# Kernel tuning notes

Hardware: AMD Instinct MI355X
Metric: run time of the kernel (lower is better)

Reference implementation:

```python
import jax, jax.numpy as jnp
import numpy as np

N = 100000   # nodes
E = 220000   # directed edges (each branch)
H = 128      # hidden_dim
OUT = 1      # output_dim
G = 4096     # num graphs in batch
PE = 5       # laplacian eigenvector PE dims
VOCAB = 28   # atom types


def gcn_conv(x, src, dst, W, b, n):
    # PyG GCNConv: x' = D^-1/2 (A + I) D^-1/2 (X W) + b
    h = x @ W
    deg = jax.ops.segment_sum(jnp.ones(src.shape[0], x.dtype), dst, num_segments=n) + 1.0
    dinv = jax.lax.rsqrt(deg)
    coef = dinv[src] * dinv[dst]                                    # [E]
    agg = jax.ops.segment_sum(h[src] * coef[:, None], dst, num_segments=n)
    agg = agg + h * (dinv * dinv)[:, None]                          # self-loop term
    return agg + b


def gcn2(x, edge_index, W1, b1, W2, b2, n):
    # PyG GCN model, num_layers=2: conv -> relu -> conv
    src, dst = edge_index[0], edge_index[1]
    h = jax.nn.relu(gcn_conv(x, src, dst, W1, b1, n))
    return gcn_conv(h, src, dst, W2, b2, n)


def setup_inputs() -> dict:
    key = jax.random.key(0)
    ks = jax.random.split(key, 16)
    s = 0.1
    return {
        "node_tokens": jax.random.randint(ks[0], (N, 1), 0, VOCAB),
        "pe": jax.random.normal(ks[1], (N, PE), jnp.float32),
        "edge_index": jax.random.randint(ks[2], (2, E), 0, N),
        "vr_edge_index": jax.random.randint(ks[3], (2, E), 0, N),
        "batch": jnp.sort(jax.random.randint(ks[4], (N,), 0, G)),
        "embed_table": jax.random.normal(ks[5], (VOCAB, H), jnp.float32) * s,
        "Wt": jax.random.normal(ks[6], (PE, H), jnp.float32) * s,
        "bt": jnp.zeros((H,), jnp.float32),
        "W1": jax.random.normal(ks[7], (H, H), jnp.float32) * s,
        "b1": jnp.zeros((H,), jnp.float32),
        "W2": jax.random.normal(ks[8], (H, OUT), jnp.float32) * s,
        "b2": jnp.zeros((OUT,), jnp.float32),
        "Wv1": jax.random.normal(ks[9], (H, H), jnp.float32) * s,
        "bv1": jnp.zeros((H,), jnp.float32),
        "Wv2": jax.random.normal(ks[10], (H, OUT), jnp.float32) * s,
        "bv2": jnp.zeros((OUT,), jnp.float32),
    }


def reference(node_tokens, pe, edge_index, vr_edge_index, batch, embed_table,
              Wt, bt, W1, b1, W2, b2, Wv1, bv1, Wv2, bv2):
    # embed_x(data.x.long()).squeeze(1) + lin_trans(pe)
    x = embed_table[node_tokens[:, 0]] + (pe @ Wt + bt)             # [N, H]
    x1 = gcn2(x, edge_index, W1, b1, W2, b2, N)                     # [N, OUT]
    xv = gcn2(x, vr_edge_index, Wv1, bv1, Wv2, bv2, N)              # [N, OUT]
    x1 = x1 + xv
    y_hat = jax.ops.segment_sum(x1, batch, num_segments=G)          # [G, OUT]
    y_hat = jnp.squeeze(y_hat, axis=-1)                             # [G]
    return (y_hat, x)
```

## Files before the change

### kernel.cpp

```cpp
#include <hip/hip_runtime.h>

#define NN 100000
#define NE 220000
#define HD 128
#define NG 4096
#define NPE 5
#define NB_SCAN ((NN + 255) / 256)
#define NBX4 ((NN * HD / 4) / 256)
#define NBF ((NN + 127) / 128)
#define NBW 128
#define NBZ ((2 * NN + 255) / 256)
#define NBE2 14
#define NBD ((2 * NE + 255) / 256)
#define LDP 136

typedef unsigned int uint;
typedef unsigned short ushort;
typedef __attribute__((ext_vector_type(8))) short bf16x8;
typedef __attribute__((ext_vector_type(4))) float f32x4;

__device__ __forceinline__ float bf2f(uint u16) {
    return __uint_as_float(u16 << 16);
}
__device__ __forceinline__ ushort f2bf(float f) {
    uint u = __float_as_uint(f);
    u += 0x7fffu + ((u >> 16) & 1u);
    return (ushort)(u >> 16);
}

__global__ void k_prep0(const float* __restrict__ W1, const float* __restrict__ Wv1,
                        const float* __restrict__ embed, const float* __restrict__ bt,
                        ushort* __restrict__ Wcat, int* __restrict__ cnt,
                        float* __restrict__ embed2) {
    int b = blockIdx.x;
    if (b < NBW) {
        int t = b * 256 + threadIdx.x;
        int f = t >> 7, k = t & 127;
        const float* W = (f < HD) ? W1 : Wv1;
        Wcat[t] = f2bf(W[k * HD + (f & 127)]);
    } else if (b < NBW + NBZ) {
        int t = (b - NBW) * 256 + threadIdx.x;
        if (t < 2 * NN) cnt[t] = 0;
    } else {
        int t = (b - NBW - NBZ) * 256 + threadIdx.x;
        if (t < 28 * 128) embed2[t] = embed[t] + bt[t & 127];
    }
}

__global__ void k_front(const int* __restrict__ tok, const float* __restrict__ pe,
                        const float* __restrict__ embed2, const float* __restrict__ Wtr,
                        float* __restrict__ x, ushort* __restrict__ xb,
                        const int* __restrict__ ei, const int* __restrict__ vei,
                        int* __restrict__ cnt) {
    int b = blockIdx.x;
    if (b < NBX4) {
        int idx = b * 256 + threadIdx.x;
        int n = idx >> 5, q = idx & 31;
        int t = tok[n];
        float4 acc = ((const float4*)(embed2 + (size_t)t * HD))[q];
        const float* pen = pe + n * NPE;
#pragma unroll
        for (int k = 0; k < NPE; ++k) {
            float p = pen[k];
            float4 wv = ((const float4*)(Wtr + k * HD))[q];
            acc.x += p * wv.x; acc.y += p * wv.y;
            acc.z += p * wv.z; acc.w += p * wv.w;
        }
        ((float4*)x)[idx] = acc;
        uint2 pk;
        pk.x = (uint)f2bf(acc.x) | ((uint)f2bf(acc.y) << 16);
        pk.y = (uint)f2bf(acc.z) | ((uint)f2bf(acc.w) << 16);
        ((uint2*)xb)[idx] = pk;
    } else {
        int t = (b - NBX4) * 256 + threadIdx.x;
        if (t < 2 * NE) {
            int br = t >= NE;
            int e = t - br * NE;
            const int* S = br ? vei : ei;
            atomicAdd(&cnt[br * NN + S[NE + e]], 1);
        }
    }
}

__global__ __launch_bounds__(256) void k_gemm(const ushort* __restrict__ xb,
                                              const ushort* __restrict__ Wt,
                                              ushort* __restrict__ H) {
    __shared__ ushort As[128 * LDP];
    int bi = blockIdx.x;
    int fh = bi >= NBF;
    int n0 = (bi - fh * NBF) * 128;
    int tid = threadIdx.x;
    {
        uint4* dst = (uint4*)As;
        for (int i = tid; i < 2048; i += 256) {
            int n = n0 + (i >> 4);
            uint4 v = {0u, 0u, 0u, 0u};
            if (n < NN) v = ((const uint4*)(xb + (size_t)n * HD))[i & 15];
            dst[(i >> 4) * 17 + (i & 15)] = v;
        }
    }
    __syncthreads();
    int w = tid >> 6, lane = tid & 63;
    int m = lane & 15, quad = lane >> 4;
    const ushort* Wg = Wt + (size_t)fh * 128 * 128;
    f32x4 acc[2][8] = {};
#pragma unroll
    for (int kc = 0; kc < 4; ++kc) {
        int k0 = kc * 32 + quad * 8;
        bf16x8 xf[2];
#pragma unroll
        for (int nt = 0; nt < 2; ++nt)
            xf[nt] = *(const bf16x8*)&As[((w * 2 + nt) * 16 + m) * LDP + k0];
#pragma unroll
        for (int ft = 0; ft < 8; ++ft) {
            bf16x8 wf = *(const bf16x8*)&Wg[(ft * 16 + m) * 128 + k0];
#pragma unroll
            for (int nt = 0; nt < 2; ++nt)
                acc[nt][ft] = __builtin_amdgcn_mfma_f32_16x16x32_bf16(
                    wf, xf[nt], acc[nt][ft], 0, 0, 0);
        }
    }
#pragma unroll
    for (int nt = 0; nt < 2; ++nt) {
        int n = n0 + (w * 2 + nt) * 16 + m;
        if (n >= NN) continue;
#pragma unroll
        for (int ft = 0; ft < 8; ++ft) {
            f32x4 a = acc[nt][ft];
            uint2 pk;
            pk.x = (uint)f2bf(a[0]) | ((uint)f2bf(a[1]) << 16);
            pk.y = (uint)f2bf(a[2]) | ((uint)f2bf(a[3]) << 16);
            *(uint2*)&H[(size_t)n * 256 + fh * 128 + ft * 16 + quad * 4] = pk;
        }
    }
}

__global__ void k_scan1(const int* __restrict__ cnt, int* __restrict__ off,
                        int* __restrict__ bsum, float* __restrict__ dinv,
                        float* __restrict__ y) {
    __shared__ int s[256];
    int tid = threadIdx.x;
    int gid = blockIdx.x * 256 + tid;
    if (gid < NG) y[gid] = 0.f;
    int br = blockIdx.x / NB_SCAN;
    int blk = blockIdx.x % NB_SCAN;
    int i = blk * 256 + tid;
    int v = (i < NN) ? cnt[br * NN + i] : 0;
    if (i < NN) dinv[br * NN + i] = rsqrtf((float)v + 1.0f);
    s[tid] = v;
    __syncthreads();
    for (int d = 1; d < 256; d <<= 1) {
        int t = (tid >= d) ? s[tid - d] : 0;
        __syncthreads();
        s[tid] += t;
        __syncthreads();
    }
    if (i < NN) off[br * NN + i] = s[tid] - v;
    if (tid == 255) bsum[br * 512 + blk] = s[255];
}

__global__ void k_scan2(int* __restrict__ bsum) {
    __shared__ int s[512];
    int br = blockIdx.x;
    int tid = threadIdx.x;
    int v = (tid < NB_SCAN) ? bsum[br * 512 + tid] : 0;
    s[tid] = v;
    __syncthreads();
    for (int d = 1; d < 512; d <<= 1) {
        int t = (tid >= d) ? s[tid - d] : 0;
        __syncthreads();
        s[tid] += t;
        __syncthreads();
    }
    if (tid < NB_SCAN) bsum[br * 512 + tid] = s[tid] - v;
}

__global__ void k_scan3(const int* __restrict__ off, const int* __restrict__ bsum,
                        const int* __restrict__ cnt, int2* __restrict__ off2,
                        int* __restrict__ cur) {
    int br = blockIdx.x / NB_SCAN;
    int blk = blockIdx.x % NB_SCAN;
    int i = blk * 256 + threadIdx.x;
    if (i < NN) {
        int o = off[br * NN + i] + bsum[br * 512 + blk];
        int2 pr;
        pr.x = o;
        pr.y = o + cnt[br * NN + i];
        off2[br * NN + i] = pr;
        cur[br * NN + i] = o;
    }
}

__global__ void k_scatter(const int* __restrict__ ei, const int* __restrict__ vei,
                          const float* __restrict__ dinv, int* __restrict__ cur,
                          int2* __restrict__ ent) {
    int t = blockIdx.x * blockDim.x + threadIdx.x;
    if (t >= 2 * NE) return;
    int br = t >= NE;
    int e = t - br * NE;
    const int* S = br ? vei : ei;
    int s = S[e], d = S[NE + e];
    int pos = atomicAdd(&cur[br * NN + d], 1);
    int2 rec;
    rec.x = s;
    rec.y = __float_as_int(dinv[br * NN + s] * dinv[br * NN + d]);
    ent[br * NE + pos] = rec;
}

__global__ void k_gather_ep(const ushort* __restrict__ H, const float* __restrict__ dinv,
                            const int2* __restrict__ off2,
                            const int2* __restrict__ ent,
                            const float* __restrict__ b1, const float* __restrict__ bv1,
                            const float* __restrict__ W2, const float* __restrict__ Wv2,
                            float* __restrict__ z) {
    int wid = threadIdx.x >> 6;
    int lane = threadIdx.x & 63;
    int half = lane >> 5;
    int l = lane & 31;
    int task = blockIdx.x * 8 + wid * 2 + half;
    int br = task >= NN;
    int n = task - br * NN;

    const int2* en = ent + br * NE;
    size_t hoff = (size_t)br * 128;

    float dv = dinv[br * NN + n];
    uint2 u = *(const uint2*)(H + (size_t)n * 256 + hoff + l * 4);
    float c = dv * dv;
    float a0 = bf2f(u.x & 0xffffu) * c, a1 = bf2f(u.x >> 16) * c;
    float a2 = bf2f(u.y & 0xffffu) * c, a3 = bf2f(u.y >> 16) * c;

    int2 pr = off2[br * NN + n];
    int p0 = pr.x, p1 = pr.y;
    for (int p = p0; p < p1; p += 4) {
        int2 e0 = en[p], e1 = en[p + 1], e2 = en[p + 2], e3 = en[p + 3];
        int s0 = e0.x;
        int s1 = (p + 1 < p1) ? e1.x : n;
        int s2 = (p + 2 < p1) ? e2.x : n;
        int s3 = (p + 3 < p1) ? e3.x : n;
        float c0 = __int_as_float(e0.y);
        float c1 = (p + 1 < p1) ? __int_as_float(e1.y) : 0.f;
        float c2 = (p + 2 < p1) ? __int_as_float(e2.y) : 0.f;
        float c3 = (p + 3 < p1) ? __int_as_float(e3.y) : 0.f;
        uint2 v0 = *(const uint2*)(H + (size_t)s0 * 256 + hoff + l * 4);
        uint2 v1 = *(const uint2*)(H + (size_t)s1 * 256 + hoff + l * 4);
        uint2 v2 = *(const uint2*)(H + (size_t)s2 * 256 + hoff + l * 4);
        uint2 v3 = *(const uint2*)(H + (size_t)s3 * 256 + hoff + l * 4);
        a0 += bf2f(v0.x & 0xffffu) * c0; a1 += bf2f(v0.x >> 16) * c0;
        a2 += bf2f(v0.y & 0xffffu) * c0; a3 += bf2f(v0.y >> 16) * c0;
        a0 += bf2f(v1.x & 0xffffu) * c1; a1 += bf2f(v1.x >> 16) * c1;
        a2 += bf2f(v1.y & 0xffffu) * c1; a3 += bf2f(v1.y >> 16) * c1;
        a0 += bf2f(v2.x & 0xffffu) * c2; a1 += bf2f(v2.x >> 16) * c2;
        a2 += bf2f(v2.y & 0xffffu) * c2; a3 += bf2f(v2.y >> 16) * c2;
        a0 += bf2f(v3.x & 0xffffu) * c3; a1 += bf2f(v3.x >> 16) * c3;
        a2 += bf2f(v3.y & 0xffffu) * c3; a3 += bf2f(v3.y >> 16) * c3;
    }

    const float* bb = br ? bv1 : b1;
    const float* ww = br ? Wv2 : W2;
    float4 b4 = *(const float4*)&bb[l * 4];
    float4 w4 = *(const float4*)&ww[l * 4];
    float part = fmaxf(a0 + b4.x, 0.f) * w4.x + fmaxf(a1 + b4.y, 0.f) * w4.y
               + fmaxf(a2 + b4.z, 0.f) * w4.z + fmaxf(a3 + b4.w, 0.f) * w4.w;
#pragma unroll
    for (int o = 16; o > 0; o >>= 1) part += __shfl_down(part, o, 32);
    if (l == 0) z[br * NN + n] = part;
}

__global__ void k_final2(const float* __restrict__ z, const float* __restrict__ dinv,
                         const int2* __restrict__ off2,
                         const int2* __restrict__ ent,
                         const float* __restrict__ b2, const float* __restrict__ bv2,
                         const int* __restrict__ batch, float* __restrict__ y) {
    __shared__ float ybuf[256];
    __shared__ int gbase_s;
    int br = blockIdx.x >= NB_SCAN;
    int nb = blockIdx.x - br * NB_SCAN;
    int tid = threadIdx.x;
    ybuf[tid] = 0.f;
    if (tid == 0) gbase_s = batch[nb * 256];
    __syncthreads();
    int gbase = gbase_s;
    int n = nb * 256 + tid;
    if (n < NN) {
        const int2* en = ent + br * NE;
        float dv = dinv[br * NN + n];
        float acc = z[br * NN + n] * dv * dv;
        int2 pr = off2[br * NN + n];
        int p1 = pr.y;
        for (int p = pr.x; p < p1; p += 4) {
            int2 e0 = en[p], e1 = en[p + 1], e2 = en[p + 2], e3 = en[p + 3];
            int s0 = e0.x;
            int s1 = (p + 1 < p1) ? e1.x : n;
            int s2 = (p + 2 < p1) ? e2.x : n;
            int s3 = (p + 3 < p1) ? e3.x : n;
            float c0 = __int_as_float(e0.y);
            float c1 = (p + 1 < p1) ? __int_as_float(e1.y) : 0.f;
            float c2 = (p + 2 < p1) ? __int_as_float(e2.y) : 0.f;
            float c3 = (p + 3 < p1) ? __int_as_float(e3.y) : 0.f;
            acc += c0 * z[br * NN + s0] + c1 * z[br * NN + s1]
                 + c2 * z[br * NN + s2] + c3 * z[br * NN + s3];
        }
        acc += br ? bv2[0] : b2[0];
        int gi = batch[n] - gbase;
        if (gi < 256) atomicAdd(&ybuf[gi], acc);
        else atomicAdd(&y[batch[n]], acc);
    }
    __syncthreads();
    float v = ybuf[tid];
    if (v != 0.f) atomicAdd(&y[gbase + tid], v);
}

extern "C" void kernel_launch(void* const* d_in, const int* in_sizes, int n_in,
                              void* d_out, int out_size, void* d_ws, size_t ws_size,
                              hipStream_t stream) {
    const int*   tok   = (const int*)d_in[0];
    const float* pe    = (const float*)d_in[1];
    const int*   ei    = (const int*)d_in[2];
    const int*   vei   = (const int*)d_in[3];
    const int*   batch = (const int*)d_in[4];
    const float* embed = (const float*)d_in[5];
    const float* Wtr   = (const float*)d_in[6];
    const float* bt    = (const float*)d_in[7];
    const float* W1    = (const float*)d_in[8];
    const float* b1    = (const float*)d_in[9];
    const float* W2    = (const float*)d_in[10];
    const float* b2    = (const float*)d_in[11];
    const float* Wv1   = (const float*)d_in[12];
    const float* bv1   = (const float*)d_in[13];
    const float* Wv2   = (const float*)d_in[14];
    const float* bv2   = (const float*)d_in[15];

    float* y = (float*)d_out;
    float* x = y + NG;

    char* w = (char*)d_ws;
    ushort* xb   = (ushort*)w;               w += (size_t)NN * HD * 2;
    ushort* H    = (ushort*)w;               w += (size_t)NN * 256 * 2;
    ushort* Wcat = (ushort*)w;               w += 256 * 128 * 2;
    float*  emb2 = (float*)w;                w += 28 * 128 * 4;
    float*  dinv = (float*)w;                w += 2 * NN * 4;
    float*  z    = (float*)w;                w += 2 * NN * 4;
    int*    cnt  = (int*)w;                  w += 2 * NN * 4;
    int*    off  = (int*)w;                  w += 2 * NN * 4;
    int*    cur  = (int*)w;                  w += 2 * NN * 4;
    int2*   off2 = (int2*)w;                 w += (size_t)2 * NN * 8;
    int2*   ent  = (int2*)w;                 w += (size_t)(2 * NE + 8) * 8;
    int*    bsum = (int*)w;                  w += 2 * 512 * 4;

    k_prep0<<<NBW + NBZ + NBE2, 256, 0, stream>>>(W1, Wv1, embed, bt, Wcat, cnt, emb2);
    k_front<<<NBX4 + NBD, 256, 0, stream>>>(tok, pe, emb2, Wtr, x, xb, ei, vei, cnt);
    k_gemm<<<2 * NBF, 256, 0, stream>>>(xb, Wcat, H);
    k_scan1<<<2 * NB_SCAN, 256, 0, stream>>>(cnt, off, bsum, dinv, y);
    k_scan2<<<2, 512, 0, stream>>>(bsum);
    k_scan3<<<2 * NB_SCAN, 256, 0, stream>>>(off, bsum, cnt, off2, cur);
    k_scatter<<<NBD, 256, 0, stream>>>(ei, vei, dinv, cur, ent);
    k_gather_ep<<<2 * NN / 8, 256, 0, stream>>>(H, dinv, off2, ent,
                                                b1, bv1, W2, Wv2, z);
    k_final2<<<2 * NB_SCAN, 256, 0, stream>>>(z, dinv, off2, ent,
                                              b2, bv2, batch, y);
}
```

Baseline: 255.5 us.

## Load GEMM operands directly from global and fold block-sum scan into scan3

The bf16 GEMM no longer stages activation rows through shared memory. Each wave now loads its 16-row A fragments directly from global memory, and blocks shrink to 64 rows, which doubles the grid. Separately, the k_scan2 launch is removed: each k_scan3 block reduces the preceding block sums itself in shared memory. This saves a kernel launch and a serial dependency, at the cost of every block re-reading up to 391 partial sums.

```diff
diff --git a/kernel.cpp b/kernel.cpp
--- a/kernel.cpp
+++ b/kernel.cpp
@@ -7,12 +7,11 @@
 #define NPE 5
 #define NB_SCAN ((NN + 255) / 256)
 #define NBX4 ((NN * HD / 4) / 256)
-#define NBF ((NN + 127) / 128)
+#define NBG ((NN + 63) / 64)
 #define NBW 128
 #define NBZ ((2 * NN + 255) / 256)
 #define NBE2 14
 #define NBD ((2 * NE + 255) / 256)
-#define LDP 136
 
 typedef unsigned int uint;
 typedef unsigned short ushort;
@@ -85,48 +84,33 @@
 __global__ __launch_bounds__(256) void k_gemm(const ushort* __restrict__ xb,
                                               const ushort* __restrict__ Wt,
                                               ushort* __restrict__ H) {
-    __shared__ ushort As[128 * LDP];
     int bi = blockIdx.x;
-    int fh = bi >= NBF;
-    int n0 = (bi - fh * NBF) * 128;
+    int fh = bi >= NBG;
+    int b = bi - fh * NBG;
     int tid = threadIdx.x;
-    {
-        uint4* dst = (uint4*)As;
-        for (int i = tid; i < 2048; i += 256) {
-            int n = n0 + (i >> 4);
-            uint4 v = {0u, 0u, 0u, 0u};
-            if (n < NN) v = ((const uint4*)(xb + (size_t)n * HD))[i & 15];
-            dst[(i >> 4) * 17 + (i & 15)] = v;
-        }
-    }
-    __syncthreads();
     int w = tid >> 6, lane = tid & 63;
     int m = lane & 15, quad = lane >> 4;
-    const ushort* Wg = Wt + (size_t)fh * 128 * 128;
-    f32x4 acc[2][8] = {};
-#pragma unroll
-    for (int kc = 0; kc < 4; ++kc) {
-        int k0 = kc * 32 + quad * 8;
-        bf16x8 xf[2];
-#pragma unroll
-        for (int nt = 0; nt < 2; ++nt)
-            xf[nt] = *(const bf16x8*)&As[((w * 2 + nt) * 16 + m) * LDP + k0];
+    int n = b * 64 + w * 16 + m;
+    int nc = (n < NN) ? n : (NN - 1);
+    const ushort* Arow = xb + (size_t)nc * HD + quad * 8;
+    const ushort* Wg = Wt + (size_t)fh * 128 * 128 + (size_t)m * 128 + quad * 8;
+    bf16x8 xf[4];
+#pragma unroll
+    for (int kc = 0; kc < 4; ++kc)
+        xf[kc] = *(const bf16x8*)(Arow + kc * 32);
+    f32x4 acc[8] = {};
+#pragma unroll
+    for (int ft = 0; ft < 8; ++ft) {
+#pragma unroll
+        for (int kc = 0; kc < 4; ++kc) {
+            bf16x8 wf = *(const bf16x8*)(Wg + (size_t)ft * 16 * 128 + kc * 32);
+            acc[ft] = __builtin_amdgcn_mfma_f32_16x16x32_bf16(wf, xf[kc], acc[ft], 0, 0, 0);
+        }
+    }
+    if (n < NN) {
 #pragma unroll
         for (int ft = 0; ft < 8; ++ft) {
-            bf16x8 wf = *(const bf16x8*)&Wg[(ft * 16 + m) * 128 + k0];
-#pragma unroll
-            for (int nt = 0; nt < 2; ++nt)
-                acc[nt][ft] = __builtin_amdgcn_mfma_f32_16x16x32_bf16(
-                    wf, xf[nt], acc[nt][ft], 0, 0, 0);
-        }
-    }
-#pragma unroll
-    for (int nt = 0; nt < 2; ++nt) {
-        int n = n0 + (w * 2 + nt) * 16 + m;
-        if (n >= NN) continue;
-#pragma unroll
-        for (int ft = 0; ft < 8; ++ft) {
-            f32x4 a = acc[nt][ft];
+            f32x4 a = acc[ft];
             uint2 pk;
             pk.x = (uint)f2bf(a[0]) | ((uint)f2bf(a[1]) << 16);
             pk.y = (uint)f2bf(a[2]) | ((uint)f2bf(a[3]) << 16);
@@ -159,30 +143,27 @@
     if (tid == 255) bsum[br * 512 + blk] = s[255];
 }
 
-__global__ void k_scan2(int* __restrict__ bsum) {
-    __shared__ int s[512];
-    int br = blockIdx.x;
-    int tid = threadIdx.x;
-    int v = (tid < NB_SCAN) ? bsum[br * 512 + tid] : 0;
-    s[tid] = v;
-    __syncthreads();
-    for (int d = 1; d < 512; d <<= 1) {
-        int t = (tid >= d) ? s[tid - d] : 0;
-        __syncthreads();
-        s[tid] += t;
-        __syncthreads();
-    }
-    if (tid < NB_SCAN) bsum[br * 512 + tid] = s[tid] - v;
-}
-
 __global__ void k_scan3(const int* __restrict__ off, const int* __restrict__ bsum,
                         const int* __restrict__ cnt, int2* __restrict__ off2,
                         int* __restrict__ cur) {
+    __shared__ int s[256];
     int br = blockIdx.x / NB_SCAN;
     int blk = blockIdx.x % NB_SCAN;
-    int i = blk * 256 + threadIdx.x;
+    int tid = threadIdx.x;
+    int v = 0;
+    if (tid < blk) v = bsum[br * 512 + tid];
+    if (tid + 256 < blk) v += bsum[br * 512 + tid + 256];
+    s[tid] = v;
+#pragma unroll
+    for (int d = 128; d > 0; d >>= 1) {
+        __syncthreads();
+        if (tid < d) s[tid] += s[tid + d];
+    }
+    __syncthreads();
+    int pre = s[0];
+    int i = blk * 256 + tid;
     if (i < NN) {
-        int o = off[br * NN + i] + bsum[br * 512 + blk];
+        int o = off[br * NN + i] + pre;
         int2 pr;
         pr.x = o;
         pr.y = o + cnt[br * NN + i];
@@ -350,9 +331,8 @@
 
     k_prep0<<<NBW + NBZ + NBE2, 256, 0, stream>>>(W1, Wv1, embed, bt, Wcat, cnt, emb2);
     k_front<<<NBX4 + NBD, 256, 0, stream>>>(tok, pe, emb2, Wtr, x, xb, ei, vei, cnt);
-    k_gemm<<<2 * NBF, 256, 0, stream>>>(xb, Wcat, H);
+    k_gemm<<<2 * NBG, 256, 0, stream>>>(xb, Wcat, H);
     k_scan1<<<2 * NB_SCAN, 256, 0, stream>>>(cnt, off, bsum, dinv, y);
-    k_scan2<<<2, 512, 0, stream>>>(bsum);
     k_scan3<<<2 * NB_SCAN, 256, 0, stream>>>(off, bsum, cnt, off2, cur);
     k_scatter<<<NBD, 256, 0, stream>>>(ei, vei, dinv, cur, ent);
     k_gather_ep<<<2 * NN / 8, 256, 0, stream>>>(H, dinv, off2, ent,
```

Result: slower. 262.1 us (+2.6%).
